# Kernel tuning notes

Measured on AMD Instinct MI355X. Metric: run time of the kernel, lower is better.

The kernel has to match this reference:

```python
import jax, jax.numpy as jnp
import numpy as np

VOCAB, EMBED, HIDDEN, BATCH, SEQ = 32000, 512, 1024, 64, 512


def _xavier(key, shape):
    fan_out, fan_in = shape
    limit = float(np.sqrt(6.0 / (fan_in + fan_out)))
    return jax.random.uniform(key, shape, jnp.float32, -limit, limit)


def setup_inputs() -> dict:
    key = jax.random.key(0)
    ks = jax.random.split(key, 12)
    inp = {
        "texts": jax.random.randint(ks[0], (BATCH, SEQ), 0, VOCAB, dtype=jnp.int32),
        "emb": jax.random.normal(ks[1], (VOCAB, EMBED), jnp.float32),
        # layer 0: input_dim = EMBED
        "Wf0": _xavier(ks[2], (HIDDEN, EMBED + HIDDEN)), "bf0": jnp.zeros((HIDDEN,), jnp.float32),
        "Wi0": _xavier(ks[3], (HIDDEN, EMBED + HIDDEN)), "bi0": jnp.zeros((HIDDEN,), jnp.float32),
        "Wo0": _xavier(ks[4], (HIDDEN, EMBED + HIDDEN)), "bo0": jnp.zeros((HIDDEN,), jnp.float32),
        "Wc0": _xavier(ks[5], (HIDDEN, EMBED + HIDDEN)), "bc0": jnp.zeros((HIDDEN,), jnp.float32),
        # layer 1: input_dim = HIDDEN
        "Wf1": _xavier(ks[6], (HIDDEN, 2 * HIDDEN)), "bf1": jnp.zeros((HIDDEN,), jnp.float32),
        "Wi1": _xavier(ks[7], (HIDDEN, 2 * HIDDEN)), "bi1": jnp.zeros((HIDDEN,), jnp.float32),
        "Wo1": _xavier(ks[8], (HIDDEN, 2 * HIDDEN)), "bo1": jnp.zeros((HIDDEN,), jnp.float32),
        "Wc1": _xavier(ks[9], (HIDDEN, 2 * HIDDEN)), "bc1": jnp.zeros((HIDDEN,), jnp.float32),
        "Wy": _xavier(ks[10], (VOCAB, HIDDEN)), "by": jnp.zeros((VOCAB,), jnp.float32),
    }
    return inp


def _lstm_layer(xs, Wf, bf, Wi, bi, Wo, bo, Wc, bc):
    # xs: (T, B, F). torch.cat((h, x), dim=0) -> weight cols are [h | x].
    B = xs.shape[1]
    H = Wf.shape[0]
    h0 = jnp.zeros((B, H), xs.dtype)
    c0 = jnp.zeros((B, H), xs.dtype)

    def step(carry, x):
        h, c = carry
        concat = jnp.concatenate([h, x], axis=1)  # (B, H+F)
        ft = jax.nn.sigmoid(concat @ Wf.T + bf)
        it = jax.nn.sigmoid(concat @ Wi.T + bi)
        c_hat = jnp.tanh(concat @ Wc.T + bc)
        c = ft * c + it * c_hat
        ot = jax.nn.sigmoid(concat @ Wo.T + bo)
        h = ot * jnp.tanh(c)
        return (h, c), h

    (_, _), hs = jax.lax.scan(step, (h0, c0), xs)
    return hs  # (T, B, H)


def reference(texts, emb, Wf0, bf0, Wi0, bi0, Wo0, bo0, Wc0, bc0,
              Wf1, bf1, Wi1, bi1, Wo1, bo1, Wc1, bc1, Wy, by):
    # embedded: (T, B, E)
    xs = jnp.transpose(emb[texts], (1, 0, 2))
    hs0 = _lstm_layer(xs, Wf0, bf0, Wi0, bi0, Wo0, bo0, Wc0, bc0)
    hs1 = _lstm_layer(hs0, Wf1, bf1, Wi1, bi1, Wo1, bo1, Wc1, bc1)
    h_last = hs1[-1]  # (B, H) = last timestep of last layer (finetune=True branch)
    y = h_last @ Wy.T + by  # (B, VOCAB); .squeeze(1) in torch is a no-op for VOCAB>1
    return y
```

## Files before the change

kernel.cpp:

```cpp
#include <hip/hip_runtime.h>
#include <stdint.h>
#include <stddef.h>

#define T_SEQ  512
#define NBATCH 64
#define EMBED  512
#define HIDDEN 1024
#define VOCAB  32000
#define NWG    256
#define NTHR   256
#define AGENT  __HIP_MEMORY_SCOPE_AGENT
#define RING   260
#define SLOT_E (NBATCH * 2048)

#define RST   66
#define BUFH  (32 * RST)

typedef __attribute__((ext_vector_type(8))) short short8;
typedef __attribute__((ext_vector_type(4))) float f32x4;

__device__ __forceinline__ unsigned short f2bf(float x) {
  union { float f; unsigned u; } v; v.f = x;
  unsigned r = v.u + 0x7FFFu + ((v.u >> 16) & 1u);
  return (unsigned short)(r >> 16);
}
__device__ __forceinline__ float sigm(float x) { return 1.0f / (1.0f + __expf(-x)); }
__device__ __forceinline__ float tanh_(float x) {
  float e = __expf(2.0f * x);
  return 1.0f - 2.0f / (e + 1.0f);
}

__global__ void embed_k(const int* __restrict__ texts, const float* __restrict__ emb,
                        unsigned short* __restrict__ xs) {
  const int bid = blockIdx.x;
  const int t = bid >> 6, b = bid & 63;
  const int row = texts[b * T_SEQ + t];
  const float* src = emb + (size_t)row * EMBED;
  const int e = threadIdx.x * 2;
  float2 v = *(const float2*)(src + e);
  unsigned pk = (unsigned)f2bf(v.x) | ((unsigned)f2bf(v.y) << 16);
  *(unsigned*)(xs + (size_t)bid * EMBED + e) = pk;
}

__device__ __forceinline__ void gbar_(unsigned* bar, unsigned ep, int tid, int g16) {
  __syncthreads();
  if (tid == 0) {
    unsigned old = __hip_atomic_fetch_add(bar + g16 * 32, 1u, __ATOMIC_RELAXED, AGENT);
    if (old == 16u * ep - 1u) {
      unsigned o2 = __hip_atomic_fetch_add(bar + 512, 1u, __ATOMIC_RELAXED, AGENT);
      if (o2 == 16u * ep - 1u)
        __hip_atomic_store(bar + 544, ep, __ATOMIC_RELAXED, AGENT);
    }
    while (__hip_atomic_load(bar + 544, __ATOMIC_RELAXED, AGENT) < ep)
      __builtin_amdgcn_s_sleep(1);
  }
  __syncthreads();
  __builtin_amdgcn_fence(__ATOMIC_ACQUIRE, "workgroup");
  asm volatile("" ::: "memory");
}

template<int XDIM, int LAG>
__device__ __forceinline__ void run_layer(
    const unsigned short* __restrict__ xs_all,
    unsigned short* __restrict__ state,
    unsigned* __restrict__ bar,
    const float* __restrict__ W0, const float* __restrict__ W1,
    const float* __restrict__ W2, const float* __restrict__ W3,
    const float* __restrict__ B0, const float* __restrict__ B1,
    const float* __restrict__ B2, const float* __restrict__ B3,
    float* buf, int wl, int gw, int tid)
{
  constexpr int K  = HIDDEN + XDIM;
  constexpr int KT = K / 128;
  const int lane = tid & 63;
  const int wid  = tid >> 6;
  const int ln   = lane & 15;
  const int qq   = lane >> 4;
  const int d0   = (tid & 3) * 2;
  const int b    = tid >> 2;
  const int gk0  = wl * 8 + d0;
  const int kbase = wid * (KT * 32);
  const int g16  = gw >> 4;
  unsigned ep = 0;

  short8 wreg[KT][2];
  #pragma unroll
  for (int m = 0; m < 2; ++m) {
    const int r = m * 16 + ln;
    const int g = r >> 3;
    const float* Wp = (g == 0) ? W0 : (g == 1) ? W1 : (g == 2) ? W2 : W3;
    const float* row = Wp + (size_t)(wl * 8 + (r & 7)) * K;
    #pragma unroll
    for (int kt = 0; kt < KT; ++kt) {
      const int kk = kbase + kt * 32 + qq * 8;
      f32x4 lo = *(const f32x4*)(row + kk);
      f32x4 hi = *(const f32x4*)(row + kk + 4);
      short8 v;
      v[0] = (short)f2bf(lo[0]); v[1] = (short)f2bf(lo[1]);
      v[2] = (short)f2bf(lo[2]); v[3] = (short)f2bf(lo[3]);
      v[4] = (short)f2bf(hi[0]); v[5] = (short)f2bf(hi[1]);
      v[6] = (short)f2bf(hi[2]); v[7] = (short)f2bf(hi[3]);
      wreg[kt][m] = v;
    }
  }

  {
    unsigned* su = (unsigned*)state;
    const int idx = gw * NTHR + tid;
    __hip_atomic_store(su + idx, 0u, __ATOMIC_RELAXED, AGENT);
    __hip_atomic_store(su + 65536 + idx, 0u, __ATOMIC_RELAXED, AGENT);
  }

  const float bsf0 = B0[gk0], bsf1 = B0[gk0 + 1];
  const float bsi0 = B1[gk0], bsi1 = B1[gk0 + 1];
  const float bso0 = B2[gk0], bso1 = B2[gk0 + 1];
  const float bsc0 = B3[gk0], bsc1 = B3[gk0 + 1];
  float c0 = 0.0f, c1 = 0.0f;

  gbar_(bar, ++ep, tid, g16);

  for (int s = 0; s <= T_SEQ; ++s) {
    const int t = s - LAG;
    if (t >= 0 && t < T_SEQ) {
      const int so  = s % RING;
      const int so1 = (s + 1) % RING;
      const unsigned short* slotS = state + (size_t)so * SLOT_E;
      const unsigned short* xrow = nullptr;
      if constexpr (XDIM == EMBED)
        xrow = xs_all + (size_t)t * (NBATCH * EMBED);

      f32x4 acc[2][4] = {};
      #pragma unroll
      for (int kt = 0; kt < KT; ++kt) {
        const int kk = kbase + kt * 32 + qq * 8;
        const unsigned short* src;
        int str, col;
        if constexpr (XDIM == HIDDEN) {
          src = slotS; str = 2048; col = kk;
        } else {
          const bool hid = (kbase + kt * 32) < HIDDEN;
          src = hid ? (slotS + 1024) : xrow;
          str = hid ? 2048 : EMBED;
          col = hid ? kk : (kk - HIDDEN);
        }
        short8 bf[4];
        #pragma unroll
        for (int nt = 0; nt < 4; ++nt)
          bf[nt] = *(const short8*)(src + (size_t)(nt * 16 + ln) * str + col);
        #pragma unroll
        for (int mt = 0; mt < 2; ++mt)
          #pragma unroll
          for (int nt = 0; nt < 4; ++nt)
            acc[mt][nt] = __builtin_amdgcn_mfma_f32_16x16x32_bf16(
                wreg[kt][mt], bf[nt], acc[mt][nt], 0, 0, 0);
      }

      if (wid < 2) {
        float* bb = buf + wid * BUFH;
        #pragma unroll
        for (int mt = 0; mt < 2; ++mt)
          #pragma unroll
          for (int nt = 0; nt < 4; ++nt)
            #pragma unroll
            for (int j = 0; j < 4; ++j)
              bb[(mt * 16 + qq * 4 + j) * RST + nt * 16 + ln] = acc[mt][nt][j];
      }
      __syncthreads();
      if (wid >= 2) {
        float* bb = buf + (wid - 2) * BUFH;
        #pragma unroll
        for (int mt = 0; mt < 2; ++mt)
          #pragma unroll
          for (int nt = 0; nt < 4; ++nt)
            #pragma unroll
            for (int j = 0; j < 4; ++j)
              bb[(mt * 16 + qq * 4 + j) * RST + nt * 16 + ln] += acc[mt][nt][j];
      }
      __syncthreads();

      {
        const float gf0 = buf[(0  + d0) * RST + b] + buf[BUFH + (0  + d0) * RST + b] + bsf0;
        const float gf1 = buf[(1  + d0) * RST + b] + buf[BUFH + (1  + d0) * RST + b] + bsf1;
        const float gi0 = buf[(8  + d0) * RST + b] + buf[BUFH + (8  + d0) * RST + b] + bsi0;
        const float gi1 = buf[(9  + d0) * RST + b] + buf[BUFH + (9  + d0) * RST + b] + bsi1;
        const float go0 = buf[(16 + d0) * RST + b] + buf[BUFH + (16 + d0) * RST + b] + bso0;
        const float go1 = buf[(17 + d0) * RST + b] + buf[BUFH + (17 + d0) * RST + b] + bso1;
        const float gc0 = buf[(24 + d0) * RST + b] + buf[BUFH + (24 + d0) * RST + b] + bsc0;
        const float gc1 = buf[(25 + d0) * RST + b] + buf[BUFH + (25 + d0) * RST + b] + bsc1;
        c0 = sigm(gf0) * c0 + sigm(gi0) * tanh_(gc0);
        c1 = sigm(gf1) * c1 + sigm(gi1) * tanh_(gc1);
        const float h0 = sigm(go0) * tanh_(c0);
        const float h1 = sigm(go1) * tanh_(c1);
        const unsigned pk = (unsigned)f2bf(h0) | ((unsigned)f2bf(h1) << 16);
        const size_t oe = (size_t)so1 * SLOT_E + (size_t)b * 2048
                        + (XDIM == EMBED ? 1024 : 0) + gk0;
        __hip_atomic_store((unsigned*)state + (oe >> 1), pk, __ATOMIC_RELAXED, AGENT);
      }
    }
    gbar_(bar, ++ep, tid, g16);
  }
}

__launch_bounds__(NTHR, 1)
__global__ void lstm_k(const unsigned short* __restrict__ xs,
                       unsigned short* __restrict__ state,
                       unsigned* __restrict__ bar,
                       const float* __restrict__ Wf0, const float* __restrict__ Wi0,
                       const float* __restrict__ Wo0, const float* __restrict__ Wc0,
                       const float* __restrict__ bf0, const float* __restrict__ bi0,
                       const float* __restrict__ bo0, const float* __restrict__ bc0,
                       const float* __restrict__ Wf1, const float* __restrict__ Wi1,
                       const float* __restrict__ Wo1, const float* __restrict__ Wc1,
                       const float* __restrict__ bf1, const float* __restrict__ bi1,
                       const float* __restrict__ bo1, const float* __restrict__ bc1)
{
  __shared__ __align__(16) float buf[2 * BUFH];
  const int tid = threadIdx.x;
  const int gw = blockIdx.x;
  if (gw < 128)
    run_layer<EMBED, 0>(xs, state, bar, Wf0, Wi0, Wo0, Wc0,
                        bf0, bi0, bo0, bc0, buf, gw, gw, tid);
  else
    run_layer<HIDDEN, 1>(nullptr, state, bar, Wf1, Wi1, Wo1, Wc1,
                         bf1, bi1, bo1, bc1, buf, gw - 128, gw, tid);
}

__global__ void final_k(const float* __restrict__ Wy,
                        const unsigned short* __restrict__ hlast,
                        const float* __restrict__ by,
                        float* __restrict__ out)
{
  const int tid = threadIdx.x, lane = tid & 63, wid = tid >> 6;
  const int ln = lane & 15, qq = lane >> 4;
  const int vbase = (blockIdx.x * 4 + wid) * 16;
  f32x4 acc[4] = {};
  const float* arow = Wy + (size_t)(vbase + ln) * HIDDEN;
  for (int kt = 0; kt < 32; ++kt) {
    const int kk = kt * 32 + qq * 8;
    f32x4 lo = *(const f32x4*)(arow + kk);
    f32x4 hi = *(const f32x4*)(arow + kk + 4);
    short8 a;
    a[0] = (short)f2bf(lo[0]); a[1] = (short)f2bf(lo[1]);
    a[2] = (short)f2bf(lo[2]); a[3] = (short)f2bf(lo[3]);
    a[4] = (short)f2bf(hi[0]); a[5] = (short)f2bf(hi[1]);
    a[6] = (short)f2bf(hi[2]); a[7] = (short)f2bf(hi[3]);
    #pragma unroll
    for (int nt = 0; nt < 4; ++nt) {
      short8 bv = *(const short8*)(hlast + (size_t)(nt * 16 + ln) * 2048 + kk);
      acc[nt] = __builtin_amdgcn_mfma_f32_16x16x32_bf16(a, bv, acc[nt], 0, 0, 0);
    }
  }
  const int v0 = vbase + qq * 4;
  const f32x4 bias = *(const f32x4*)(by + v0);
  #pragma unroll
  for (int nt = 0; nt < 4; ++nt) {
    const int bb = nt * 16 + ln;
    f32x4 r = acc[nt] + bias;
    *(f32x4*)(out + (size_t)bb * VOCAB + v0) = r;
  }
}

extern "C" void kernel_launch(void* const* d_in, const int* in_sizes, int n_in,
                              void* d_out, int out_size, void* d_ws, size_t ws_size,
                              hipStream_t stream) {
  (void)in_sizes; (void)n_in; (void)out_size; (void)ws_size;
  const int*   texts = (const int*)d_in[0];
  const float* emb   = (const float*)d_in[1];
  const float* Wf0 = (const float*)d_in[2];  const float* bf0 = (const float*)d_in[3];
  const float* Wi0 = (const float*)d_in[4];  const float* bi0 = (const float*)d_in[5];
  const float* Wo0 = (const float*)d_in[6];  const float* bo0 = (const float*)d_in[7];
  const float* Wc0 = (const float*)d_in[8];  const float* bc0 = (const float*)d_in[9];
  const float* Wf1 = (const float*)d_in[10]; const float* bf1 = (const float*)d_in[11];
  const float* Wi1 = (const float*)d_in[12]; const float* bi1 = (const float*)d_in[13];
  const float* Wo1 = (const float*)d_in[14]; const float* bo1 = (const float*)d_in[15];
  const float* Wc1 = (const float*)d_in[16]; const float* bc1 = (const float*)d_in[17];
  const float* Wy  = (const float*)d_in[18]; const float* by  = (const float*)d_in[19];

  char* ws = (char*)d_ws;
  unsigned*       bar   = (unsigned*)ws;
  unsigned short* state = (unsigned short*)(ws + 4096);
  unsigned short* xs    = (unsigned short*)(ws + 4096 + (size_t)RING * SLOT_E * 2);
  float* out = (float*)d_out;

  hipMemsetAsync(bar, 0, 4096, stream);
  embed_k<<<T_SEQ * NBATCH, 256, 0, stream>>>(texts, emb, xs);
  lstm_k<<<NWG, NTHR, 0, stream>>>(xs, state, bar,
                                   Wf0, Wi0, Wo0, Wc0, bf0, bi0, bo0, bc0,
                                   Wf1, Wi1, Wo1, Wc1, bf1, bi1, bo1, bc1);
  final_k<<<VOCAB / 64, 256, 0, stream>>>(
      Wy, state + (size_t)((T_SEQ + 1) % RING) * SLOT_E, by, out);
}
```

Baseline: 5.152 ms.

## Replace global barrier with per-timestep counters and halve workgroup count

Swaps the grid-wide barrier used every step for per-layer, per-timestep arrival counters. Each workgroup waits only on the specific step it depends on, so layer 0 can run ahead of layer 1 within a bounded ring lag, and layer 0 computes its input projection before waiting for the recurrent state. The grid drops from 256 to 128 workgroups, each owning 16 hidden units across all four gates with a 4-way K split reduced through shared memory. This cuts barrier latency and allows cross-layer pipelining, at the cost of more register-resident weights per workgroup and fewer CUs doing the recurrent matmul.

```diff
diff --git a/kernel.cpp b/kernel.cpp
--- a/kernel.cpp
+++ b/kernel.cpp
@@ -7,14 +7,17 @@
 #define EMBED  512
 #define HIDDEN 1024
 #define VOCAB  32000
-#define NWG    256
+#define NWG    128
 #define NTHR   256
 #define AGENT  __HIP_MEMORY_SCOPE_AGENT
 #define RING   260
 #define SLOT_E (NBATCH * 2048)
+#define BOUND  250
 
 #define RST   66
-#define BUFH  (32 * RST)
+#define PBUF  (64 * RST)
+
+#define CNT(l, t) (cnt + ((((t) << 1) | (l)) << 5))
 
 typedef __attribute__((ext_vector_type(8))) short short8;
 typedef __attribute__((ext_vector_type(4))) float f32x4;
@@ -28,6 +31,13 @@
 __device__ __forceinline__ float tanh_(float x) {
   float e = __expf(2.0f * x);
   return 1.0f - 2.0f / (e + 1.0f);
+}
+
+__device__ __forceinline__ void wait_ge(unsigned* p, unsigned tgt) {
+  while (__hip_atomic_load(p, __ATOMIC_RELAXED, AGENT) < tgt)
+    __builtin_amdgcn_s_sleep(1);
+  __builtin_amdgcn_fence(__ATOMIC_ACQUIRE, "workgroup");
+  asm volatile("" ::: "memory");
 }
 
 __global__ void embed_k(const int* __restrict__ texts, const float* __restrict__ emb,
@@ -42,169 +52,169 @@
   *(unsigned*)(xs + (size_t)bid * EMBED + e) = pk;
 }
 
-__device__ __forceinline__ void gbar_(unsigned* bar, unsigned ep, int tid, int g16) {
-  __syncthreads();
-  if (tid == 0) {
-    unsigned old = __hip_atomic_fetch_add(bar + g16 * 32, 1u, __ATOMIC_RELAXED, AGENT);
-    if (old == 16u * ep - 1u) {
-      unsigned o2 = __hip_atomic_fetch_add(bar + 512, 1u, __ATOMIC_RELAXED, AGENT);
-      if (o2 == 16u * ep - 1u)
-        __hip_atomic_store(bar + 544, ep, __ATOMIC_RELAXED, AGENT);
-    }
-    while (__hip_atomic_load(bar + 544, __ATOMIC_RELAXED, AGENT) < ep)
-      __builtin_amdgcn_s_sleep(1);
-  }
-  __syncthreads();
-  __builtin_amdgcn_fence(__ATOMIC_ACQUIRE, "workgroup");
-  asm volatile("" ::: "memory");
-}
-
-template<int XDIM, int LAG>
+template<int LAYER>
 __device__ __forceinline__ void run_layer(
     const unsigned short* __restrict__ xs_all,
     unsigned short* __restrict__ state,
-    unsigned* __restrict__ bar,
+    unsigned* __restrict__ cnt,
     const float* __restrict__ W0, const float* __restrict__ W1,
     const float* __restrict__ W2, const float* __restrict__ W3,
     const float* __restrict__ B0, const float* __restrict__ B1,
     const float* __restrict__ B2, const float* __restrict__ B3,
-    float* buf, int wl, int gw, int tid)
+    float* buf, int w, int tid)
 {
-  constexpr int K  = HIDDEN + XDIM;
+  constexpr int K  = LAYER ? 2048 : 1536;
   constexpr int KT = K / 128;
   const int lane = tid & 63;
   const int wid  = tid >> 6;
   const int ln   = lane & 15;
   const int qq   = lane >> 4;
-  const int d0   = (tid & 3) * 2;
-  const int b    = tid >> 2;
-  const int gk0  = wl * 8 + d0;
-  const int kbase = wid * (KT * 32);
-  const int g16  = gw >> 4;
-  unsigned ep = 0;
-
-  short8 wreg[KT][2];
+  const int d0   = (tid & 7) * 2;
+  const int bp   = (tid >> 3) * 2;
+  const int gk0  = w * 16 + d0;
+
+  short8 wreg[KT][4];
+  const float* Wg[4] = {W0, W1, W2, W3};
   #pragma unroll
-  for (int m = 0; m < 2; ++m) {
-    const int r = m * 16 + ln;
-    const int g = r >> 3;
-    const float* Wp = (g == 0) ? W0 : (g == 1) ? W1 : (g == 2) ? W2 : W3;
-    const float* row = Wp + (size_t)(wl * 8 + (r & 7)) * K;
+  for (int mt = 0; mt < 4; ++mt) {
+    const float* row = Wg[mt] + (size_t)(w * 16 + ln) * K;
     #pragma unroll
     for (int kt = 0; kt < KT; ++kt) {
-      const int kk = kbase + kt * 32 + qq * 8;
-      f32x4 lo = *(const f32x4*)(row + kk);
-      f32x4 hi = *(const f32x4*)(row + kk + 4);
+      int col;
+      if (LAYER == 1) col = wid * 512 + kt * 32;
+      else col = (kt < 4) ? (1024 + wid * 128 + kt * 32) : (wid * 256 + (kt - 4) * 32);
+      col += qq * 8;
+      f32x4 lo = *(const f32x4*)(row + col);
+      f32x4 hi = *(const f32x4*)(row + col + 4);
       short8 v;
       v[0] = (short)f2bf(lo[0]); v[1] = (short)f2bf(lo[1]);
       v[2] = (short)f2bf(lo[2]); v[3] = (short)f2bf(lo[3]);
       v[4] = (short)f2bf(hi[0]); v[5] = (short)f2bf(hi[1]);
       v[6] = (short)f2bf(hi[2]); v[7] = (short)f2bf(hi[3]);
-      wreg[kt][m] = v;
-    }
-  }
-
-  {
-    unsigned* su = (unsigned*)state;
-    const int idx = gw * NTHR + tid;
-    __hip_atomic_store(su + idx, 0u, __ATOMIC_RELAXED, AGENT);
-    __hip_atomic_store(su + 65536 + idx, 0u, __ATOMIC_RELAXED, AGENT);
-  }
-
-  const float bsf0 = B0[gk0], bsf1 = B0[gk0 + 1];
-  const float bsi0 = B1[gk0], bsi1 = B1[gk0 + 1];
-  const float bso0 = B2[gk0], bso1 = B2[gk0 + 1];
-  const float bsc0 = B3[gk0], bsc1 = B3[gk0 + 1];
-  float c0 = 0.0f, c1 = 0.0f;
-
-  gbar_(bar, ++ep, tid, g16);
-
-  for (int s = 0; s <= T_SEQ; ++s) {
-    const int t = s - LAG;
-    if (t >= 0 && t < T_SEQ) {
-      const int so  = s % RING;
-      const int so1 = (s + 1) % RING;
-      const unsigned short* slotS = state + (size_t)so * SLOT_E;
-      const unsigned short* xrow = nullptr;
-      if constexpr (XDIM == EMBED)
-        xrow = xs_all + (size_t)t * (NBATCH * EMBED);
-
-      f32x4 acc[2][4] = {};
-      #pragma unroll
-      for (int kt = 0; kt < KT; ++kt) {
-        const int kk = kbase + kt * 32 + qq * 8;
-        const unsigned short* src;
-        int str, col;
-        if constexpr (XDIM == HIDDEN) {
-          src = slotS; str = 2048; col = kk;
-        } else {
-          const bool hid = (kbase + kt * 32) < HIDDEN;
-          src = hid ? (slotS + 1024) : xrow;
-          str = hid ? 2048 : EMBED;
-          col = hid ? kk : (kk - HIDDEN);
-        }
+      wreg[kt][mt] = v;
+    }
+  }
+
+  float bs[4][2];
+  #pragma unroll
+  for (int g = 0; g < 4; ++g) {
+    const float* Bg = (g == 0) ? B0 : (g == 1) ? B1 : (g == 2) ? B2 : B3;
+    bs[g][0] = Bg[gk0]; bs[g][1] = Bg[gk0 + 1];
+  }
+  float cst[2][2] = {{0.f, 0.f}, {0.f, 0.f}};
+
+  wait_ge(CNT(0, 512), NWG);
+
+  for (int t = 0; t < T_SEQ; ++t) {
+    const int so  = t % RING;
+    const int so1 = (t + 1) % RING;
+    const unsigned short* slotT  = state + (size_t)so  * SLOT_E;
+    const unsigned short* slotT1 = state + (size_t)so1 * SLOT_E;
+    f32x4 acc[4][4] = {};
+
+    if constexpr (LAYER == 0) {
+      const unsigned short* xrow = xs_all + (size_t)t * (NBATCH * EMBED);
+      #pragma unroll
+      for (int kt = 0; kt < 4; ++kt) {
+        const int bc = wid * 128 + kt * 32 + qq * 8;
         short8 bf[4];
         #pragma unroll
         for (int nt = 0; nt < 4; ++nt)
-          bf[nt] = *(const short8*)(src + (size_t)(nt * 16 + ln) * str + col);
-        #pragma unroll
-        for (int mt = 0; mt < 2; ++mt)
+          bf[nt] = *(const short8*)(xrow + (size_t)(nt * 16 + ln) * EMBED + bc);
+        #pragma unroll
+        for (int mt = 0; mt < 4; ++mt)
           #pragma unroll
           for (int nt = 0; nt < 4; ++nt)
             acc[mt][nt] = __builtin_amdgcn_mfma_f32_16x16x32_bf16(
                 wreg[kt][mt], bf[nt], acc[mt][nt], 0, 0, 0);
       }
-
-      if (wid < 2) {
-        float* bb = buf + wid * BUFH;
-        #pragma unroll
-        for (int mt = 0; mt < 2; ++mt)
+      if (t > 0) wait_ge(CNT(0, t - 1), 64);
+      const unsigned short* hbase = slotT + 1024;
+      #pragma unroll
+      for (int kt = 4; kt < KT; ++kt) {
+        const int hc = wid * 256 + (kt - 4) * 32 + qq * 8;
+        short8 bf[4];
+        #pragma unroll
+        for (int nt = 0; nt < 4; ++nt)
+          bf[nt] = *(const short8*)(hbase + (size_t)(nt * 16 + ln) * 2048 + hc);
+        #pragma unroll
+        for (int mt = 0; mt < 4; ++mt)
           #pragma unroll
           for (int nt = 0; nt < 4; ++nt)
-            #pragma unroll
-            for (int j = 0; j < 4; ++j)
-              bb[(mt * 16 + qq * 4 + j) * RST + nt * 16 + ln] = acc[mt][nt][j];
+            acc[mt][nt] = __builtin_amdgcn_mfma_f32_16x16x32_bf16(
+                wreg[kt][mt], bf[nt], acc[mt][nt], 0, 0, 0);
       }
-      __syncthreads();
-      if (wid >= 2) {
-        float* bb = buf + (wid - 2) * BUFH;
-        #pragma unroll
-        for (int mt = 0; mt < 2; ++mt)
+    } else {
+      if (wid >= 2)      wait_ge(CNT(0, t), 64);
+      else if (t > 0)    wait_ge(CNT(1, t - 1), 64);
+      const unsigned short* base = (wid < 2) ? slotT : slotT1;
+      #pragma unroll
+      for (int kt = 0; kt < KT; ++kt) {
+        const int c = wid * 512 + kt * 32 + qq * 8;
+        short8 bf[4];
+        #pragma unroll
+        for (int nt = 0; nt < 4; ++nt)
+          bf[nt] = *(const short8*)(base + (size_t)(nt * 16 + ln) * 2048 + c);
+        #pragma unroll
+        for (int mt = 0; mt < 4; ++mt)
           #pragma unroll
           for (int nt = 0; nt < 4; ++nt)
-            #pragma unroll
-            for (int j = 0; j < 4; ++j)
-              bb[(mt * 16 + qq * 4 + j) * RST + nt * 16 + ln] += acc[mt][nt][j];
+            acc[mt][nt] = __builtin_amdgcn_mfma_f32_16x16x32_bf16(
+                wreg[kt][mt], bf[nt], acc[mt][nt], 0, 0, 0);
       }
-      __syncthreads();
-
-      {
-        const float gf0 = buf[(0  + d0) * RST + b] + buf[BUFH + (0  + d0) * RST + b] + bsf0;
-        const float gf1 = buf[(1  + d0) * RST + b] + buf[BUFH + (1  + d0) * RST + b] + bsf1;
-        const float gi0 = buf[(8  + d0) * RST + b] + buf[BUFH + (8  + d0) * RST + b] + bsi0;
-        const float gi1 = buf[(9  + d0) * RST + b] + buf[BUFH + (9  + d0) * RST + b] + bsi1;
-        const float go0 = buf[(16 + d0) * RST + b] + buf[BUFH + (16 + d0) * RST + b] + bso0;
-        const float go1 = buf[(17 + d0) * RST + b] + buf[BUFH + (17 + d0) * RST + b] + bso1;
-        const float gc0 = buf[(24 + d0) * RST + b] + buf[BUFH + (24 + d0) * RST + b] + bsc0;
-        const float gc1 = buf[(25 + d0) * RST + b] + buf[BUFH + (25 + d0) * RST + b] + bsc1;
-        c0 = sigm(gf0) * c0 + sigm(gi0) * tanh_(gc0);
-        c1 = sigm(gf1) * c1 + sigm(gi1) * tanh_(gc1);
-        const float h0 = sigm(go0) * tanh_(c0);
-        const float h1 = sigm(go1) * tanh_(c1);
-        const unsigned pk = (unsigned)f2bf(h0) | ((unsigned)f2bf(h1) << 16);
-        const size_t oe = (size_t)so1 * SLOT_E + (size_t)b * 2048
-                        + (XDIM == EMBED ? 1024 : 0) + gk0;
-        __hip_atomic_store((unsigned*)state + (oe >> 1), pk, __ATOMIC_RELAXED, AGENT);
+    }
+
+    {
+      float* bb = buf + wid * PBUF;
+      #pragma unroll
+      for (int mt = 0; mt < 4; ++mt)
+        #pragma unroll
+        for (int nt = 0; nt < 4; ++nt)
+          #pragma unroll
+          for (int j = 0; j < 4; ++j)
+            bb[(mt * 16 + qq * 4 + j) * RST + nt * 16 + ln] = acc[mt][nt][j];
+    }
+    __syncthreads();
+
+    float gv[4][2][2];
+    #pragma unroll
+    for (int gt = 0; gt < 4; ++gt)
+      #pragma unroll
+      for (int dd = 0; dd < 2; ++dd) {
+        float sx = bs[gt][dd], sy = bs[gt][dd];
+        #pragma unroll
+        for (int p = 0; p < 4; ++p) {
+          float2 v = *(const float2*)&buf[p * PBUF + (gt * 16 + d0 + dd) * RST + bp];
+          sx += v.x; sy += v.y;
+        }
+        gv[gt][dd][0] = sx; gv[gt][dd][1] = sy;
       }
-    }
-    gbar_(bar, ++ep, tid, g16);
+
+    if (LAYER == 0 && t >= BOUND)
+      wait_ge(CNT(1, t - BOUND), 64);
+
+    unsigned* su = (unsigned*)state;
+    const size_t obase = (size_t)so1 * SLOT_E + (LAYER == 0 ? 1024 : 0) + gk0;
+    #pragma unroll
+    for (int s2 = 0; s2 < 2; ++s2) {
+      cst[0][s2] = sigm(gv[0][0][s2]) * cst[0][s2] + sigm(gv[1][0][s2]) * tanh_(gv[3][0][s2]);
+      cst[1][s2] = sigm(gv[0][1][s2]) * cst[1][s2] + sigm(gv[1][1][s2]) * tanh_(gv[3][1][s2]);
+      const float h0v = sigm(gv[2][0][s2]) * tanh_(cst[0][s2]);
+      const float h1v = sigm(gv[2][1][s2]) * tanh_(cst[1][s2]);
+      const unsigned pk = (unsigned)f2bf(h0v) | ((unsigned)f2bf(h1v) << 16);
+      __hip_atomic_store(su + ((obase + (size_t)(bp + s2) * 2048) >> 1), pk,
+                         __ATOMIC_RELAXED, AGENT);
+    }
+    __syncthreads();
+    if (tid == 0)
+      __hip_atomic_fetch_add(CNT(LAYER, t), 1u, __ATOMIC_RELAXED, AGENT);
   }
 }
 
 __launch_bounds__(NTHR, 1)
 __global__ void lstm_k(const unsigned short* __restrict__ xs,
                        unsigned short* __restrict__ state,
-                       unsigned* __restrict__ bar,
+                       unsigned* __restrict__ cnt,
                        const float* __restrict__ Wf0, const float* __restrict__ Wi0,
                        const float* __restrict__ Wo0, const float* __restrict__ Wc0,
                        const float* __restrict__ bf0, const float* __restrict__ bi0,
@@ -214,15 +224,26 @@
                        const float* __restrict__ bf1, const float* __restrict__ bi1,
                        const float* __restrict__ bo1, const float* __restrict__ bc1)
 {
-  __shared__ __align__(16) float buf[2 * BUFH];
+  __shared__ __align__(16) float buf[4 * PBUF];
   const int tid = threadIdx.x;
-  const int gw = blockIdx.x;
-  if (gw < 128)
-    run_layer<EMBED, 0>(xs, state, bar, Wf0, Wi0, Wo0, Wc0,
-                        bf0, bi0, bo0, bc0, buf, gw, gw, tid);
+  const int gw  = blockIdx.x;
+
+  {
+    unsigned* su = (unsigned*)state;
+    const int idx = gw * NTHR + tid;
+    __hip_atomic_store(su + idx,         0u, __ATOMIC_RELAXED, AGENT);
+    __hip_atomic_store(su + 32768 + idx, 0u, __ATOMIC_RELAXED, AGENT);
+    __syncthreads();
+    if (tid == 0)
+      __hip_atomic_fetch_add(CNT(0, 512), 1u, __ATOMIC_RELAXED, AGENT);
+  }
+
+  if (gw < 64)
+    run_layer<0>(xs, state, cnt, Wf0, Wi0, Wo0, Wc0, bf0, bi0, bo0, bc0,
+                 buf, gw, tid);
   else
-    run_layer<HIDDEN, 1>(nullptr, state, bar, Wf1, Wi1, Wo1, Wc1,
-                         bf1, bi1, bo1, bc1, buf, gw - 128, gw, tid);
+    run_layer<1>(nullptr, state, cnt, Wf1, Wi1, Wo1, Wc1, bf1, bi1, bo1, bc1,
+                 buf, gw - 64, tid);
 }
 
 __global__ void final_k(const float* __restrict__ Wy,
@@ -277,16 +298,16 @@
   const float* Wy  = (const float*)d_in[18]; const float* by  = (const float*)d_in[19];
 
   char* ws = (char*)d_ws;
-  unsigned*       bar   = (unsigned*)ws;
-  unsigned short* state = (unsigned short*)(ws + 4096);
-  unsigned short* xs    = (unsigned short*)(ws + 4096 + (size_t)RING * SLOT_E * 2);
+  unsigned*       cnt   = (unsigned*)ws;
+  unsigned short* state = (unsigned short*)(ws + 262144);
+  unsigned short* xs    = (unsigned short*)(ws + 262144 + (size_t)RING * SLOT_E * 2);
   float* out = (float*)d_out;
 
-  hipMemsetAsync(bar, 0, 4096, stream);
+  hipMemsetAsync(cnt, 0, 135168, stream);
   embed_k<<<T_SEQ * NBATCH, 256, 0, stream>>>(texts, emb, xs);
-  lstm_k<<<NWG, NTHR, 0, stream>>>(xs, state, bar,
+  lstm_k<<<NWG, NTHR, 0, stream>>>(xs, state, cnt,
                                    Wf0, Wi0, Wo0, Wc0, bf0, bi0, bo0, bc0,
                                    Wf1, Wi1, Wo1, Wc1, bf1, bi1, bo1, bc1);
   final_k<<<VOCAB / 64, 256, 0, stream>>>(
-      Wy, state + (size_t)((T_SEQ + 1) % RING) * SLOT_E, by, out);
-}
+      Wy, state + (size_t)(T_SEQ % RING) * SLOT_E, by, out);
+}
```

After: 5.326 ms. 1.03x slower.
